# Kernel optimization log

Measured on AMD Instinct MI355X. Metric: run time of the kernel, lower is better.

The kernel has to match this reference:

```python
import jax, jax.numpy as jnp
import numpy as np

V, D, NL = 50257, 768, 12
DI, DS, DC, DTR = 1536, 16, 4, 48  # d_inner, d_state, d_conv, dt_rank
B, S = 2, 1024


def _mamba_layer(x, iw, cw, cb, xw, dw, db, Alog, Dp, ow):
    # x: (B,S,D)
    xz = x @ iw.T                      # (B,S,2*DI)
    xin, z = jnp.split(xz, 2, axis=-1)
    # depthwise causal conv over sequence
    xc = jax.lax.conv_general_dilated(
        jnp.transpose(xin, (0, 2, 1)), cw[:, None, :],
        window_strides=(1,), padding=[(DC - 1, 0)],
        feature_group_count=DI, dimension_numbers=('NCL', 'OIL', 'NCL'))
    xin = jax.nn.silu(jnp.transpose(xc, (0, 2, 1)) + cb)  # (B,S,DI)
    dbl = xin @ xw.T                   # (B,S,DTR+2*DS)
    dt, Bm, Cm = dbl[..., :DTR], dbl[..., DTR:DTR + DS], dbl[..., DTR + DS:]
    dt = jax.nn.softplus(dt @ dw.T + db)  # (B,S,DI)
    A = -jnp.exp(Alog)                 # (DI,DS)

    def step(h, inp):
        dt_t, B_t, C_t, x_t = inp      # (B,DI),(B,DS),(B,DS),(B,DI)
        h = h * jnp.exp(dt_t[:, :, None] * A) + (dt_t * x_t)[:, :, None] * B_t[:, None, :]
        y = jnp.einsum('bds,bs->bd', h, C_t)
        return h, y

    h0 = jnp.zeros((x.shape[0], DI, DS), dtype=x.dtype)
    xs = (jnp.transpose(dt, (1, 0, 2)), jnp.transpose(Bm, (1, 0, 2)),
          jnp.transpose(Cm, (1, 0, 2)), jnp.transpose(xin, (1, 0, 2)))
    _, ys = jax.lax.scan(step, h0, xs)
    y = jnp.transpose(ys, (1, 0, 2)) + xin * Dp  # (B,S,DI)
    y = y * jax.nn.silu(z)
    return y @ ow.T                    # (B,S,D)


def _layernorm(x, w, b):
    mu = jnp.mean(x, axis=-1, keepdims=True)
    var = jnp.mean(jnp.square(x - mu), axis=-1, keepdims=True)
    return (x - mu) * jax.lax.rsqrt(var + 1e-5) * w + b


def setup_inputs() -> dict:
    key = jax.random.key(0)
    ks = jax.random.split(key, 10)
    s = 0.02
    input_ids = jax.random.randint(ks[0], (B, S), 0, V)
    emb = jax.random.normal(ks[1], (V, D), jnp.float32) * s
    in_proj_w = jax.random.normal(ks[2], (NL, 2 * DI, D), jnp.float32) * s
    conv_w = jax.random.normal(ks[3], (NL, DI, DC), jnp.float32) * 0.2
    conv_b = jnp.zeros((NL, DI), jnp.float32)
    x_proj_w = jax.random.normal(ks[4], (NL, DTR + 2 * DS, DI), jnp.float32) * s
    dt_proj_w = jax.random.normal(ks[5], (NL, DI, DTR), jnp.float32) * (DTR ** -0.5)
    dt_proj_b = jax.random.normal(ks[6], (NL, DI), jnp.float32) * 0.1 - 4.0
    A_log = jnp.broadcast_to(jnp.log(jnp.arange(1, DS + 1, dtype=jnp.float32)), (NL, DI, DS)) + 0.0
    D_param = jnp.ones((NL, DI), jnp.float32)
    out_proj_w = jax.random.normal(ks[7], (NL, D, DI), jnp.float32) * s
    norm_w = jnp.ones((D,), jnp.float32)
    norm_b = jnp.zeros((D,), jnp.float32)
    return {"input_ids": input_ids, "emb": emb, "in_proj_w": in_proj_w,
            "conv_w": conv_w, "conv_b": conv_b, "x_proj_w": x_proj_w,
            "dt_proj_w": dt_proj_w, "dt_proj_b": dt_proj_b, "A_log": A_log,
            "D_param": D_param, "out_proj_w": out_proj_w,
            "norm_w": norm_w, "norm_b": norm_b}


def reference(input_ids, emb, in_proj_w, conv_w, conv_b, x_proj_w, dt_proj_w,
              dt_proj_b, A_log, D_param, out_proj_w, norm_w, norm_b):
    x = emb[input_ids] * (D ** 0.5)    # (B,S,D)
    for i in range(NL):
        x = _mamba_layer(x, in_proj_w[i], conv_w[i], conv_b[i], x_proj_w[i],
                         dt_proj_w[i], dt_proj_b[i], A_log[i], D_param[i], out_proj_w[i])
    x = _layernorm(x, norm_w, norm_b)
    return x @ emb.T                   # tied lm_head: (B,S,V)
```

## Files before the change

kernel.cpp:

```cpp
#include <hip/hip_runtime.h>
#include <hip/hip_bf16.h>

#define DI 1536
#define DS 16
#define DC 4
#define DTR 48
#define NB 2
#define SL 1024
#define DM 768
#define NLAYER 12
#define VOCAB 50257
#define ROWS (NB*SL)
#define CCH 32
#define CLEN (SL/CCH)
#define NBIG (DI+32)

typedef __attribute__((ext_vector_type(8))) short bf16x8;
typedef __attribute__((ext_vector_type(4))) short short4v;
typedef __attribute__((ext_vector_type(4))) float f32x4;

__device__ inline short f2bf(float f) {
    unsigned u = __builtin_bit_cast(unsigned, f);
    unsigned r = (u + 0x7fffu + ((u >> 16) & 1u)) >> 16;
    return (short)r;
}
__device__ inline float bf2f(unsigned short u) {
    unsigned x = ((unsigned)u) << 16;
    return __builtin_bit_cast(float, x);
}

__device__ __forceinline__ void gl_lds16(const void* g, void* l) {
    __builtin_amdgcn_global_load_lds(
        (const __attribute__((address_space(1))) unsigned int*)g,
        (__attribute__((address_space(3))) unsigned int*)l, 16, 0, 0);
}

__global__ __launch_bounds__(256) void cvt3_k(
    const float* __restrict__ s0, unsigned short* __restrict__ d0, int n40,
    const float* __restrict__ s1, unsigned short* __restrict__ d1, int n41,
    const float* __restrict__ s2, unsigned short* __restrict__ d2, int n42)
{
    int i = blockIdx.x * 256 + threadIdx.x;
    const float* src; unsigned short* dst;
    if (i < n40) { src = s0; dst = d0; }
    else if (i < n40 + n41) { i -= n40; src = s1; dst = d1; }
    else if (i < n40 + n41 + n42) { i -= n40 + n41; src = s2; dst = d2; }
    else return;
    float4 v = *reinterpret_cast<const float4*>(src + (size_t)i * 4);
    short4v o;
    o[0] = f2bf(v.x); o[1] = f2bf(v.y); o[2] = f2bf(v.z); o[3] = f2bf(v.w);
    *reinterpret_cast<short4v*>(dst + (size_t)i * 4) = o;
}

__global__ __launch_bounds__(256) void wc_k(
    const float* __restrict__ dtw_all,
    const float* __restrict__ xpw_all,
    unsigned short* __restrict__ wbig)
{
    int l = blockIdx.z;
    const float* dtw = dtw_all + (size_t)l * DI * DTR;
    const float* xpw = xpw_all + (size_t)l * 80 * DI;
    unsigned short* wb = wbig + (size_t)l * NBIG * DI;
    int tid = threadIdx.x;
    if (blockIdx.y == 12) {
        if (blockIdx.x == 0) {
            for (int idx = tid; idx < 32 * DI; idx += 256) {
                int rr = idx / DI, k = idx - rr * DI;
                wb[(size_t)(DI + rr) * DI + k] =
                    (unsigned short)f2bf(xpw[(size_t)(48 + rr) * DI + k]);
            }
        }
        return;
    }
    __shared__ float sd[128 * 48];
    __shared__ float sx[48 * 128];
    int d0 = blockIdx.y * 128, k0 = blockIdx.x * 128;
    for (int idx = tid; idx < 128 * 48; idx += 256) {
        int r = idx / 48, j = idx - r * 48;
        sd[idx] = dtw[(size_t)(d0 + r) * DTR + j];
    }
    for (int idx = tid; idx < 48 * 128; idx += 256) {
        int j = idx / 128, k = idx - j * 128;
        sx[idx] = xpw[(size_t)j * DI + k0 + k];
    }
    __syncthreads();
    int tx = tid & 15, ty = tid >> 4;
    float acc[8][8] = {};
    for (int j = 0; j < 48; ++j) {
        float a[8], w[8];
        #pragma unroll
        for (int i = 0; i < 8; ++i) a[i] = sd[(ty * 8 + i) * 48 + j];
        #pragma unroll
        for (int i = 0; i < 8; ++i) w[i] = sx[j * 128 + tx * 8 + i];
        #pragma unroll
        for (int i = 0; i < 8; ++i)
            #pragma unroll
            for (int jj = 0; jj < 8; ++jj)
                acc[i][jj] += a[i] * w[jj];
    }
    for (int i = 0; i < 8; ++i)
        for (int jj = 0; jj < 8; ++jj)
            wb[(size_t)(d0 + ty * 8 + i) * DI + k0 + tx * 8 + jj] =
                (unsigned short)f2bf(acc[i][jj]);
}

__global__ __launch_bounds__(256) void embed_k(const int* __restrict__ ids,
                                               const float* __restrict__ emb,
                                               unsigned short* __restrict__ xbf) {
    int i = blockIdx.x * 256 + threadIdx.x;
    if (i >= ROWS * (DM / 4)) return;
    int row = i / (DM / 4);
    int c4 = (i - row * (DM / 4)) * 4;
    float4 v = *reinterpret_cast<const float4*>(
        &emb[(size_t)ids[row] * DM + c4]);
    const float s = 27.712812921102035f;
    short4v o;
    o[0] = f2bf(v.x * s); o[1] = f2bf(v.y * s);
    o[2] = f2bf(v.z * s); o[3] = f2bf(v.w * s);
    *reinterpret_cast<short4v*>(&xbf[(size_t)row * DM + c4]) = o;
}

template<int MT, int NBUF, int OUT, bool NTST>
__global__ __launch_bounds__(256) void gemm_bf16(
    const unsigned short* __restrict__ A, int lda,
    const unsigned short* __restrict__ W, int ldw,
    float* __restrict__ C, unsigned short* __restrict__ Cbf, int ldc,
    int GY, int N, int K,
    const float* __restrict__ bias, float* __restrict__ aux)
{
    constexpr int BKT = 32;
    constexpr int CPR = BKT / 8;
    constexpr int ACA = (MT * CPR + 255) / 256;
    constexpr int ACW = 128 * CPR / 256;
    constexpr int ISS = ACA + ACW;
    constexpr int MFR = MT / 32;
    constexpr int BUFS = (MT + 128) * BKT;
    __shared__ __align__(16) short smem[NBUF * BUFS];

    const int tid  = threadIdx.x;
    const int lane = tid & 63;
    const int wid  = tid >> 6;
    const int wr   = wid >> 1, wc = wid & 1;

    const int nwg = gridDim.x;
    const int q = nwg >> 3, rm = nwg & 7;
    const int xcd = blockIdx.x & 7, bidx = blockIdx.x >> 3;
    const int wg = (xcd < rm ? xcd * (q + 1) : rm * (q + 1) + (xcd - rm) * q) + bidx;
    const int row0 = (wg % GY) * MT;
    const int col0 = (wg / GY) * 128;

    const unsigned short* gA[ACA];
    const unsigned short* gW[ACW];
    #pragma unroll
    for (int i = 0; i < ACA; ++i) {
        int cid = i * 256 + ((MT == 32) ? (tid & 127) : tid);
        int r = cid / CPR, c = cid % CPR;
        gA[i] = A + (size_t)(row0 + r) * lda + ((c ^ ((r >> 1) & 3)) * 8);
    }
    #pragma unroll
    for (int i = 0; i < ACW; ++i) {
        int cid = i * 256 + tid;
        int r = cid / CPR, c = cid % CPR;
        int rg = col0 + r; if (rg > N - 1) rg = N - 1;
        gW[i] = W + (size_t)rg * ldw + ((c ^ ((r >> 1) & 3)) * 8);
    }

    const int arow = (MT == 32 ? wr * 16 : wr * (MT / 2)) + (lane & 15);
    const int brow = wc * 64 + (lane & 15);
    const int szA = (arow >> 1) & 3;
    const int szB = (brow >> 1) & 3;
    const int hi = lane >> 4;

    auto STAGE = [&](int buf) {
        short* As = smem + buf * BUFS;
        short* Ws = As + MT * BKT;
        #pragma unroll
        for (int i = 0; i < ACA; ++i) {
            int cbase = (MT == 32) ? ((wid & 1) * 64) : (i * 256 + wid * 64);
            gl_lds16(gA[i], &As[cbase * 8]);
            gA[i] += BKT;
        }
        #pragma unroll
        for (int i = 0; i < ACW; ++i) {
            gl_lds16(gW[i], &Ws[(i * 256 + wid * 64) * 8]);
            gW[i] += BKT;
        }
    };

    f32x4 acc[MFR][4] = {};

    const int ntiles = K / BKT;
    #pragma unroll
    for (int p = 0; p < NBUF - 1; ++p) STAGE(p);

    for (int t = 0; t < ntiles; ++t) {
        const int next = t + NBUF - 1;
        if (next < ntiles) STAGE(next % NBUF);
        int ahead = ntiles - 1 - t;
        if (ahead > NBUF - 1) ahead = NBUF - 1;
        if (NBUF >= 4 && ahead == 3)
            asm volatile("s_waitcnt vmcnt(%0)" :: "n"(3 * ISS) : "memory");
        else if (NBUF >= 3 && ahead == 2)
            asm volatile("s_waitcnt vmcnt(%0)" :: "n"(2 * ISS) : "memory");
        else if (ahead == 1)
            asm volatile("s_waitcnt vmcnt(%0)" :: "n"(ISS) : "memory");
        else if (ahead == 0)
            asm volatile("s_waitcnt vmcnt(0)" ::: "memory");
        __builtin_amdgcn_sched_barrier(0);
        __builtin_amdgcn_s_barrier();

        const short* As = smem + (t % NBUF) * BUFS;
        const short* Ws = As + MT * BKT;
        bf16x8 a[MFR], b[4];
        #pragma unroll
        for (int mf = 0; mf < MFR; ++mf)
            a[mf] = *reinterpret_cast<const bf16x8*>(
                &As[(arow + mf * 16) * BKT + ((hi ^ szA) * 8)]);
        #pragma unroll
        for (int nf = 0; nf < 4; ++nf)
            b[nf] = *reinterpret_cast<const bf16x8*>(
                &Ws[(brow + nf * 16) * BKT + ((hi ^ szB) * 8)]);
        #pragma unroll
        for (int mf = 0; mf < MFR; ++mf)
            #pragma unroll
            for (int nf = 0; nf < 4; ++nf)
                acc[mf][nf] = __builtin_amdgcn_mfma_f32_16x16x32_bf16(
                    a[mf], b[nf], acc[mf][nf], 0, 0, 0);

        __builtin_amdgcn_s_barrier();
    }

    if (OUT == 0 && NTST) {
        __syncthreads();
        float* Cs = (float*)smem;
        #pragma unroll
        for (int mf = 0; mf < MFR; ++mf) {
            __syncthreads();
            #pragma unroll
            for (int nf = 0; nf < 4; ++nf) {
                #pragma unroll
                for (int j = 0; j < 4; ++j)
                    Cs[(wr * 16 + hi * 4 + j) * 132 + wc * 64 + nf * 16 + (lane & 15)]
                        = acc[mf][nf][j];
            }
            __syncthreads();
            #pragma unroll
            for (int rr = 0; rr < 8; ++rr) {
                int lrow = wid * 8 + rr;
                int grow = row0 + (lrow < 16 ? mf * 16 + lrow
                                             : (MT / 2) + mf * 16 + (lrow - 16));
                #pragma unroll
                for (int hf = 0; hf < 2; ++hf) {
                    int cc = col0 + hf * 64 + lane;
                    if (cc < N)
                        __builtin_nontemporal_store(
                            Cs[lrow * 132 + hf * 64 + lane],
                            &C[(size_t)grow * ldc + cc]);
                }
            }
        }
    } else {
        #pragma unroll
        for (int mf = 0; mf < MFR; ++mf) {
            #pragma unroll
            for (int nf = 0; nf < 4; ++nf) {
                int r  = row0 + (MT == 32 ? wr * 16 : wr * (MT / 2)) + mf * 16 + hi * 4;
                int cc = col0 + wc * 64 + nf * 16 + (lane & 15);
                if (cc < N) {
                    f32x4 d = acc[mf][nf];
                    if (OUT == 3) {
                        if (cc < DI) {
                            float bv = bias[cc];
                            #pragma unroll
                            for (int j = 0; j < 4; ++j) {
                                float v = d[j] + bv;
                                v = (v > 20.f) ? v : log1pf(__expf(v));
                                Cbf[(size_t)(r + j) * ldc + cc] = (unsigned short)f2bf(v);
                            }
                        } else {
                            #pragma unroll
                            for (int j = 0; j < 4; ++j)
                                aux[(size_t)(r + j) * 32 + (cc - DI)] = d[j];
                        }
                    } else if (OUT == 2) {
                        #pragma unroll
                        for (int j = 0; j < 4; ++j)
                            Cbf[(size_t)(r + j) * ldc + cc] = (unsigned short)f2bf(d[j]);
                    } else {
                        #pragma unroll
                        for (int j = 0; j < 4; ++j)
                            C[(size_t)(r + j) * ldc + cc] = d[j];
                    }
                }
            }
        }
    }
}

__global__ __launch_bounds__(256) void conv_silu_k(
    const unsigned short* __restrict__ xz, const float* __restrict__ cw,
    const float* __restrict__ cb, unsigned short* __restrict__ xinb)
{
    int i = blockIdx.x * 256 + threadIdx.x;
    if (i >= ROWS * (DI / 8)) return;
    int row = i / (DI / 8);
    int c = (i - row * (DI / 8)) * 8;
    int t = row & (SL - 1);
    int b = row >> 10;

    float4 wv[8];
    float accv[8];
    #pragma unroll
    for (int j = 0; j < 8; ++j) {
        wv[j] = *reinterpret_cast<const float4*>(&cw[(c + j) * DC]);
        accv[j] = cb[c + j];
    }
    const unsigned short* base = xz + ((size_t)(b * SL)) * (2 * DI) + c;
    #pragma unroll
    for (int k = 0; k < DC; ++k) {
        int tt = t + k - (DC - 1);
        if (tt >= 0) {
            bf16x8 v = *reinterpret_cast<const bf16x8*>(
                &base[(size_t)tt * (2 * DI)]);
            #pragma unroll
            for (int j = 0; j < 8; ++j)
                accv[j] += bf2f((unsigned short)v[j]) *
                           reinterpret_cast<const float*>(&wv[j])[k];
        }
    }
    bf16x8 o;
    #pragma unroll
    for (int j = 0; j < 8; ++j) {
        float v = accv[j] / (1.f + __expf(-accv[j]));
        o[j] = f2bf(v);
    }
    *reinterpret_cast<bf16x8*>(&xinb[(size_t)row * DI + c]) = o;
}

__global__ __launch_bounds__(256) void scan_phase1(
    const unsigned short* __restrict__ dt,
    const float* __restrict__ bc,
    const unsigned short* __restrict__ xin,
    const float* __restrict__ Alog,
    float* __restrict__ hend,
    float* __restrict__ eprod)
{
    int blk = blockIdx.x;
    int c = blk % CCH;
    int tmp = blk / CCH;
    int dblk = tmp % (DI / 16);
    int b = tmp / (DI / 16);
    int lane = threadIdx.x & 63;
    int s = lane & 15;
    int g = lane & 0x30;
    int d = dblk * 16 + (threadIdx.x >> 4);
    float A = -__expf(Alog[d * DS + s]);
    float h = 0.f, P = 1.f;
    const int rowbase = b * SL + c * CLEN;
    #pragma unroll
    for (int half = 0; half < 2; ++half) {
        int rb = rowbase + half * 16;
        int rl = rb + s;
        float dtv_b = bf2f(dt[(size_t)rl * DI + d]);
        float xv_b  = bf2f(xin[(size_t)rl * DI + d]);
        #pragma unroll
        for (int t = 0; t < 16; ++t) {
            float dtv = __shfl(dtv_b, g | t, 64);
            float xv  = __shfl(xv_b,  g | t, 64);
            float Bv  = bc[(size_t)(rb + t) * 32 + s];
            float e = __expf(dtv * A);
            h = h * e + dtv * xv * Bv;
            P *= e;
        }
    }
    size_t idx = ((size_t)(b * CCH + c) * DI + d) * DS + s;
    hend[idx]  = h;
    eprod[idx] = P;
}

__global__ __launch_bounds__(256) void scan_phase3(
    const unsigned short* __restrict__ dt,
    const float* __restrict__ bc,
    const unsigned short* __restrict__ xin,
    const unsigned short* __restrict__ xz,
    const float* __restrict__ Alog,
    const float* __restrict__ Dp,
    const float* __restrict__ hend,
    const float* __restrict__ eprod,
    unsigned short* __restrict__ ybf)
{
    int blk = blockIdx.x;
    int c = blk % CCH;
    int tmp = blk / CCH;
    int dblk = tmp % (DI / 16);
    int b = tmp / (DI / 16);
    int lane = threadIdx.x & 63;
    int s = lane & 15;
    int g = lane & 0x30;
    int d = dblk * 16 + (threadIdx.x >> 4);
    float A = -__expf(Alog[d * DS + s]);
    float Dv = Dp[d];

    float h = 0.f;
    const size_t pbase = ((size_t)b * CCH * DI + d) * DS + s;
    for (int j = 0; j < c; ++j) {
        size_t idx = pbase + (size_t)j * (DI * DS);
        h = h * eprod[idx] + hend[idx];
    }

    const int rowbase = b * SL + c * CLEN;
    #pragma unroll
    for (int half = 0; half < 2; ++half) {
        int rb = rowbase + half * 16;
        int rl = rb + s;
        float dtv_b = bf2f(dt[(size_t)rl * DI + d]);
        float xv_b  = bf2f(xin[(size_t)rl * DI + d]);
        float zv_b  = bf2f(xz[(size_t)rl * (2 * DI) + DI + d]);
        #pragma unroll
        for (int t = 0; t < 16; ++t) {
            float dtv = __shfl(dtv_b, g | t, 64);
            float xv  = __shfl(xv_b,  g | t, 64);
            int r = rb + t;
            float Bv  = bc[(size_t)r * 32 + s];
            float Cv  = bc[(size_t)r * 32 + 16 + s];
            float e = __expf(dtv * A);
            h = h * e + dtv * xv * Bv;
            float p = h * Cv;
            p += __shfl_xor(p, 1, 64);
            p += __shfl_xor(p, 2, 64);
            p += __shfl_xor(p, 4, 64);
            p += __shfl_xor(p, 8, 64);
            float z = __shfl(zv_b, g | t, 64);
            if (s == 0) {
                float yv = (p + xv * Dv) * (z / (1.f + __expf(-z)));
                ybf[(size_t)r * DI + d] = (unsigned short)f2bf(yv);
            }
        }
    }
}

__global__ __launch_bounds__(256) void ln_k(
    const unsigned short* __restrict__ x, const float* __restrict__ w,
    const float* __restrict__ b, unsigned short* __restrict__ o)
{
    int row = blockIdx.x;
    int tid = threadIdx.x;
    const unsigned short* xr = x + (size_t)row * DM;
    float v0 = bf2f(xr[tid]), v1 = bf2f(xr[tid + 256]), v2 = bf2f(xr[tid + 512]);
    float s = v0 + v1 + v2;
    #pragma unroll
    for (int off = 1; off < 64; off <<= 1) s += __shfl_xor(s, off, 64);
    __shared__ float red[4];
    __shared__ float red2[4];
    int wid = tid >> 6, lane = tid & 63;
    if (lane == 0) red[wid] = s;
    __syncthreads();
    float mu = (red[0] + red[1] + red[2] + red[3]) * (1.f / 768.f);
    float d0 = v0 - mu, d1 = v1 - mu, d2 = v2 - mu;
    float q = d0 * d0 + d1 * d1 + d2 * d2;
    #pragma unroll
    for (int off = 1; off < 64; off <<= 1) q += __shfl_xor(q, off, 64);
    if (lane == 0) red2[wid] = q;
    __syncthreads();
    float var = (red2[0] + red2[1] + red2[2] + red2[3]) * (1.f / 768.f);
    float rs = rsqrtf(var + 1e-5f);
    o[(size_t)row * DM + tid]       = (unsigned short)f2bf(d0 * rs * w[tid]       + b[tid]);
    o[(size_t)row * DM + tid + 256] = (unsigned short)f2bf(d1 * rs * w[tid + 256] + b[tid + 256]);
    o[(size_t)row * DM + tid + 512] = (unsigned short)f2bf(d2 * rs * w[tid + 512] + b[tid + 512]);
}

extern "C" void kernel_launch(void* const* d_in, const int* in_sizes, int n_in,
                              void* d_out, int out_size, void* d_ws, size_t ws_size,
                              hipStream_t stream) {
    const int*   ids        = (const int*)d_in[0];
    const float* emb        = (const float*)d_in[1];
    const float* in_proj_w  = (const float*)d_in[2];
    const float* conv_w     = (const float*)d_in[3];
    const float* conv_b     = (const float*)d_in[4];
    const float* x_proj_w   = (const float*)d_in[5];
    const float* dt_proj_w  = (const float*)d_in[6];
    const float* dt_proj_b  = (const float*)d_in[7];
    const float* A_log      = (const float*)d_in[8];
    const float* D_param    = (const float*)d_in[9];
    const float* out_proj_w = (const float*)d_in[10];
    const float* norm_w     = (const float*)d_in[11];
    const float* norm_b     = (const float*)d_in[12];
    float* out = (float*)d_out;

    char* base = (char*)d_ws;
    size_t off = 0;
    auto alloc_f = [&](size_t n) { float* p = (float*)(base + off); off += n * 4; return p; };
    auto alloc_u = [&](size_t n) { unsigned short* p = (unsigned short*)(base + off); off += n * 2; return p; };

    float* bc    = alloc_f((size_t)ROWS * 32);
    float* hend  = alloc_f((size_t)NB * CCH * DI * DS);
    float* eprod = alloc_f((size_t)NB * CCH * DI * DS);
    unsigned short* xbf   = alloc_u((size_t)ROWS * DM);
    unsigned short* xzb   = alloc_u((size_t)ROWS * 2 * DI);
    unsigned short* xinb  = alloc_u((size_t)ROWS * DI);
    unsigned short* dtbf  = alloc_u((size_t)ROWS * DI);
    unsigned short* ybf   = alloc_u((size_t)ROWS * DI);
    unsigned short* xlnbf = alloc_u((size_t)ROWS * DM);
    unsigned short* inw_bf = alloc_u((size_t)NLAYER * 2 * DI * DM);
    unsigned short* ow_bf  = alloc_u((size_t)NLAYER * DM * DI);
    unsigned short* wbig  = alloc_u((size_t)NLAYER * NBIG * DI);
    unsigned short* emb_bf = alloc_u((size_t)VOCAB * DM);
    (void)ws_size;

    {
        int n4a = NLAYER * 2 * DI * DM / 4;
        int n4b = NLAYER * DM * DI / 4;
        int n4e = VOCAB * DM / 4;
        int n4t = n4a + n4b + n4e;
        cvt3_k<<<(n4t + 255) / 256, 256, 0, stream>>>(
            in_proj_w, inw_bf, n4a, out_proj_w, ow_bf, n4b, emb, emb_bf, n4e);
        wc_k<<<dim3(12, 13, NLAYER), 256, 0, stream>>>(dt_proj_w, x_proj_w, wbig);
    }

    embed_k<<<(ROWS * (DM / 4) + 255) / 256, 256, 0, stream>>>(ids, emb, xbf);

    const int scan_grid = NB * (DI / 16) * CCH;

    for (int i = 0; i < NLAYER; ++i) {
        const float* cw  = conv_w  + (size_t)i * DI * DC;
        const float* cb  = conv_b  + (size_t)i * DI;
        const float* dtb = dt_proj_b + (size_t)i * DI;
        const float* Al  = A_log   + (size_t)i * DI * DS;
        const float* Dpar= D_param + (size_t)i * DI;

        const unsigned short* inw = inw_bf + (size_t)i * 2 * DI * DM;
        gemm_bf16<64, 4, 2, false><<<24 * 32, 256, 0, stream>>>(
            xbf, DM, inw, DM, nullptr, xzb, 2 * DI, 32, 2 * DI, DM, nullptr, nullptr);

        conv_silu_k<<<(ROWS * (DI / 8)) / 256, 256, 0, stream>>>(xzb, cw, cb, xinb);

        const unsigned short* wb = wbig + (size_t)i * NBIG * DI;
        gemm_bf16<64, 4, 3, false><<<13 * 32, 256, 0, stream>>>(
            xinb, DI, wb, DI, nullptr, dtbf, DI, 32, NBIG, DI, dtb, bc);

        scan_phase1<<<scan_grid, 256, 0, stream>>>(dtbf, bc, xinb, Al, hend, eprod);
        scan_phase3<<<scan_grid, 256, 0, stream>>>(dtbf, bc, xinb, xzb, Al, Dpar,
                                                   hend, eprod, ybf);

        const unsigned short* ow = ow_bf + (size_t)i * DM * DI;
        gemm_bf16<32, 4, 2, false><<<64 * 6, 256, 0, stream>>>(
            ybf, DI, ow, DI, nullptr, xbf, DM, 64, DM, DI, nullptr, nullptr);
    }

    ln_k<<<ROWS, 256, 0, stream>>>(xbf, norm_w, norm_b, xlnbf);
    gemm_bf16<128, 2, 0, true><<<393 * 16, 256, 0, stream>>>(
        xlnbf, DM, emb_bf, DM, out, nullptr, VOCAB, 16, VOCAB, DM, nullptr, nullptr);
}
```

Measured before the change: 2.889 ms.

## Generalize GEMM block size, use 512-thread 256-row tiles for lm_head, stage scan B/C in LDS

Templates the bf16 GEMM on block size so the vocab projection can run with 512 threads and 256-row tiles, halving the number of row tiles and re-reads of the embedding matrix. Each scan kernel also loads its chunk's B/C values into shared memory once with vector loads, replacing repeated global reads inside the sequential loop. The larger GEMM tile increases LDS and register pressure per block, and the NTST epilogue row mapping now has to handle more warp rows.

New measurement: 2.772 ms. 1.04x faster.

```diff
diff --git a/kernel.cpp b/kernel.cpp
--- a/kernel.cpp
+++ b/kernel.cpp
@@ -120,8 +120,8 @@
     *reinterpret_cast<short4v*>(&xbf[(size_t)row * DM + c4]) = o;
 }
 
-template<int MT, int NBUF, int OUT, bool NTST>
-__global__ __launch_bounds__(256) void gemm_bf16(
+template<int BS, int MT, int NBUF, int OUT, bool NTST>
+__global__ __launch_bounds__(BS) void gemm_bf16(
     const unsigned short* __restrict__ A, int lda,
     const unsigned short* __restrict__ W, int ldw,
     float* __restrict__ C, unsigned short* __restrict__ Cbf, int ldc,
@@ -130,10 +130,12 @@
 {
     constexpr int BKT = 32;
     constexpr int CPR = BKT / 8;
-    constexpr int ACA = (MT * CPR + 255) / 256;
-    constexpr int ACW = 128 * CPR / 256;
+    constexpr int WRG = (BS / 64) / 2;
+    constexpr int ACH = MT * CPR;
+    constexpr int ACA = (ACH >= BS) ? ACH / BS : 1;
+    constexpr int ACW = (128 * CPR) / BS;
     constexpr int ISS = ACA + ACW;
-    constexpr int MFR = MT / 32;
+    constexpr int MFR = MT / (16 * WRG);
     constexpr int BUFS = (MT + 128) * BKT;
     __shared__ __align__(16) short smem[NBUF * BUFS];
 
@@ -153,19 +155,19 @@
     const unsigned short* gW[ACW];
     #pragma unroll
     for (int i = 0; i < ACA; ++i) {
-        int cid = i * 256 + ((MT == 32) ? (tid & 127) : tid);
-        int r = cid / CPR, c = cid % CPR;
+        int cid = (ACH >= BS) ? (i * BS + tid) : (tid & (ACH - 1));
+        int r = cid >> 2, c = cid & 3;
         gA[i] = A + (size_t)(row0 + r) * lda + ((c ^ ((r >> 1) & 3)) * 8);
     }
     #pragma unroll
     for (int i = 0; i < ACW; ++i) {
-        int cid = i * 256 + tid;
-        int r = cid / CPR, c = cid % CPR;
+        int cid = i * BS + tid;
+        int r = cid >> 2, c = cid & 3;
         int rg = col0 + r; if (rg > N - 1) rg = N - 1;
         gW[i] = W + (size_t)rg * ldw + ((c ^ ((r >> 1) & 3)) * 8);
     }
 
-    const int arow = (MT == 32 ? wr * 16 : wr * (MT / 2)) + (lane & 15);
+    const int arow = wr * (MT / WRG) + (lane & 15);
     const int brow = wc * 64 + (lane & 15);
     const int szA = (arow >> 1) & 3;
     const int szB = (brow >> 1) & 3;
@@ -176,13 +178,14 @@
         short* Ws = As + MT * BKT;
         #pragma unroll
         for (int i = 0; i < ACA; ++i) {
-            int cbase = (MT == 32) ? ((wid & 1) * 64) : (i * 256 + wid * 64);
+            int cbase = (ACH >= BS) ? (i * BS + wid * 64)
+                                    : ((wid % (ACH / 64)) * 64);
             gl_lds16(gA[i], &As[cbase * 8]);
             gA[i] += BKT;
         }
         #pragma unroll
         for (int i = 0; i < ACW; ++i) {
-            gl_lds16(gW[i], &Ws[(i * 256 + wid * 64) * 8]);
+            gl_lds16(gW[i], &Ws[(i * BS + wid * 64) * 8]);
             gW[i] += BKT;
         }
     };
@@ -247,8 +250,8 @@
             #pragma unroll
             for (int rr = 0; rr < 8; ++rr) {
                 int lrow = wid * 8 + rr;
-                int grow = row0 + (lrow < 16 ? mf * 16 + lrow
-                                             : (MT / 2) + mf * 16 + (lrow - 16));
+                int qq = lrow >> 4, rmr = lrow & 15;
+                int grow = row0 + qq * (MT / WRG) + mf * 16 + rmr;
                 #pragma unroll
                 for (int hf = 0; hf < 2; ++hf) {
                     int cc = col0 + hf * 64 + lane;
@@ -264,7 +267,7 @@
         for (int mf = 0; mf < MFR; ++mf) {
             #pragma unroll
             for (int nf = 0; nf < 4; ++nf) {
-                int r  = row0 + (MT == 32 ? wr * 16 : wr * (MT / 2)) + mf * 16 + hi * 4;
+                int r  = row0 + wr * (MT / WRG) + mf * 16 + hi * 4;
                 int cc = col0 + wc * 64 + nf * 16 + (lane & 15);
                 if (cc < N) {
                     f32x4 d = acc[mf][nf];
@@ -354,9 +357,15 @@
     int s = lane & 15;
     int g = lane & 0x30;
     int d = dblk * 16 + (threadIdx.x >> 4);
+    const int rowbase = b * SL + c * CLEN;
+
+    __shared__ float sbc[CLEN * 32];
+    *reinterpret_cast<float4*>(&sbc[threadIdx.x * 4]) =
+        *reinterpret_cast<const float4*>(&bc[(size_t)rowbase * 32 + threadIdx.x * 4]);
     float A = -__expf(Alog[d * DS + s]);
+    __syncthreads();
+
     float h = 0.f, P = 1.f;
-    const int rowbase = b * SL + c * CLEN;
     #pragma unroll
     for (int half = 0; half < 2; ++half) {
         int rb = rowbase + half * 16;
@@ -367,7 +376,7 @@
         for (int t = 0; t < 16; ++t) {
             float dtv = __shfl(dtv_b, g | t, 64);
             float xv  = __shfl(xv_b,  g | t, 64);
-            float Bv  = bc[(size_t)(rb + t) * 32 + s];
+            float Bv  = sbc[(half * 16 + t) * 32 + s];
             float e = __expf(dtv * A);
             h = h * e + dtv * xv * Bv;
             P *= e;
@@ -398,6 +407,11 @@
     int s = lane & 15;
     int g = lane & 0x30;
     int d = dblk * 16 + (threadIdx.x >> 4);
+    const int rowbase = b * SL + c * CLEN;
+
+    __shared__ float sbc[CLEN * 32];
+    *reinterpret_cast<float4*>(&sbc[threadIdx.x * 4]) =
+        *reinterpret_cast<const float4*>(&bc[(size_t)rowbase * 32 + threadIdx.x * 4]);
     float A = -__expf(Alog[d * DS + s]);
     float Dv = Dp[d];
 
@@ -407,8 +421,8 @@
         size_t idx = pbase + (size_t)j * (DI * DS);
         h = h * eprod[idx] + hend[idx];
     }
-
-    const int rowbase = b * SL + c * CLEN;
+    __syncthreads();
+
     #pragma unroll
     for (int half = 0; half < 2; ++half) {
         int rb = rowbase + half * 16;
@@ -421,8 +435,8 @@
             float dtv = __shfl(dtv_b, g | t, 64);
             float xv  = __shfl(xv_b,  g | t, 64);
             int r = rb + t;
-            float Bv  = bc[(size_t)r * 32 + s];
-            float Cv  = bc[(size_t)r * 32 + 16 + s];
+            float Bv  = sbc[(half * 16 + t) * 32 + s];
+            float Cv  = sbc[(half * 16 + t) * 32 + 16 + s];
             float e = __expf(dtv * A);
             h = h * e + dtv * xv * Bv;
             float p = h * Cv;
@@ -529,13 +543,13 @@
         const float* Dpar= D_param + (size_t)i * DI;
 
         const unsigned short* inw = inw_bf + (size_t)i * 2 * DI * DM;
-        gemm_bf16<64, 4, 2, false><<<24 * 32, 256, 0, stream>>>(
+        gemm_bf16<256, 64, 4, 2, false><<<24 * 32, 256, 0, stream>>>(
             xbf, DM, inw, DM, nullptr, xzb, 2 * DI, 32, 2 * DI, DM, nullptr, nullptr);
 
         conv_silu_k<<<(ROWS * (DI / 8)) / 256, 256, 0, stream>>>(xzb, cw, cb, xinb);
 
         const unsigned short* wb = wbig + (size_t)i * NBIG * DI;
-        gemm_bf16<64, 4, 3, false><<<13 * 32, 256, 0, stream>>>(
+        gemm_bf16<256, 64, 4, 3, false><<<13 * 32, 256, 0, stream>>>(
             xinb, DI, wb, DI, nullptr, dtbf, DI, 32, NBIG, DI, dtb, bc);
 
         scan_phase1<<<scan_grid, 256, 0, stream>>>(dtbf, bc, xinb, Al, hend, eprod);
@@ -543,11 +557,11 @@
                                                    hend, eprod, ybf);
 
         const unsigned short* ow = ow_bf + (size_t)i * DM * DI;
-        gemm_bf16<32, 4, 2, false><<<64 * 6, 256, 0, stream>>>(
+        gemm_bf16<256, 32, 4, 2, false><<<64 * 6, 256, 0, stream>>>(
             ybf, DI, ow, DI, nullptr, xbf, DM, 64, DM, DI, nullptr, nullptr);
     }
 
     ln_k<<<ROWS, 256, 0, stream>>>(xbf, norm_w, norm_b, xlnbf);
-    gemm_bf16<128, 2, 0, true><<<393 * 16, 256, 0, stream>>>(
-        xlnbf, DM, emb_bf, DM, out, nullptr, VOCAB, 16, VOCAB, DM, nullptr, nullptr);
-}
+    gemm_bf16<512, 256, 2, 0, true><<<393 * 8, 512, 0, stream>>>(
+        xlnbf, DM, emb_bf, DM, out, nullptr, VOCAB, 8, VOCAB, DM, nullptr, nullptr);
+}
```
